# Kernel tuning notes

Measured on AMD Instinct MI355X. Metric: run time of the kernel, lower is better.

Reference implementation:

```python
import jax, jax.numpy as jnp
import numpy as np

D_MODEL = 1024
NUM_HEADS = 16
D_K = D_MODEL // NUM_HEADS
NEG = -1e9


def setup_inputs() -> dict:
    key = jax.random.key(0)
    ks = jax.random.split(key, 7)
    B, S = 2, 2048
    q = jax.random.normal(ks[0], (B, S, D_MODEL), dtype=jnp.float32)
    k = jax.random.normal(ks[1], (B, S, D_MODEL), dtype=jnp.float32)
    v = jax.random.normal(ks[2], (B, S, D_MODEL), dtype=jnp.float32)
    mask = jnp.ones((B, S), dtype=jnp.int32)
    # nn.Linear(d_model, d_model, bias=False): y = x @ W.T, W:[out,in]
    scale = 1.0 / np.sqrt(D_MODEL)
    Wq = jax.random.normal(ks[3], (D_MODEL, D_MODEL), dtype=jnp.float32) * scale
    Wk = jax.random.normal(ks[4], (D_MODEL, D_MODEL), dtype=jnp.float32) * scale
    Wv = jax.random.normal(ks[5], (D_MODEL, D_MODEL), dtype=jnp.float32) * scale
    Wo = jax.random.normal(ks[6], (D_MODEL, D_MODEL), dtype=jnp.float32) * scale
    return {"q": q, "k": k, "v": v, "mask": mask,
            "Wq": Wq, "Wk": Wk, "Wv": Wv, "Wo": Wo}


def _split_heads(x, B):
    # [B,S,D] -> [B,H,S,d_k]
    return x.reshape(B, -1, NUM_HEADS, D_K).transpose(0, 2, 1, 3)


def reference(q, k, v, mask, Wq, Wk, Wv, Wo):
    B = q.shape[0]
    qh = _split_heads(q @ Wq.T, B)
    kh = _split_heads(k @ Wk.T, B)
    vh = _split_heads(v @ Wv.T, B)
    # [B,H,Sq,Sk]
    scores = jnp.einsum('bhqd,bhkd->bhqk', qh, kh) / jnp.sqrt(jnp.float32(D_K))
    Sq, Sk = scores.shape[-2], scores.shape[-1]
    causal = jnp.triu(jnp.ones((Sq, Sk), dtype=bool), k=1)
    scores = jnp.where(causal[None, None], NEG, scores)
    pad = (mask[:, None, None, :] == 0)  # [B,1,1,Sk]
    scores = jnp.where(pad, NEG, scores)
    weights = jax.nn.softmax(scores, axis=-1)
    out = jnp.einsum('bhqk,bhkd->bhqd', weights, vh)
    out = out.transpose(0, 2, 1, 3).reshape(B, -1, D_MODEL)
    return out @ Wo.T
```

## Files before the change

### kernel.cpp

```cpp
#include <hip/hip_runtime.h>
#include <hip/hip_bf16.h>
#include <stdint.h>

using bf16 = __hip_bfloat16;
typedef __attribute__((ext_vector_type(8))) short short8;
typedef __attribute__((ext_vector_type(4))) float f32x4;
typedef __attribute__((ext_vector_type(16))) float f32x16;
typedef __attribute__((ext_vector_type(4))) float float4v;
typedef __attribute__((ext_vector_type(4))) unsigned short us4;
typedef __attribute__((ext_vector_type(4))) uint32_t u32x4;
typedef __attribute__((ext_vector_type(2))) uint32_t u32x2;

#define LDS_U32 __attribute__((address_space(3))) uint32_t
#define GLB_U32 __attribute__((address_space(1))) uint32_t

__device__ __forceinline__ unsigned short f2b(float f) {
  union { float f; uint32_t u; } x; x.f = f;
  uint32_t r = x.u + 0x7FFFu + ((x.u >> 16) & 1u);
  return (unsigned short)(r >> 16);
}

__global__ void cast_all(const float* __restrict__ q, const float* __restrict__ k,
                         const float* __restrict__ v, const float* __restrict__ Wq,
                         const float* __restrict__ Wk, const float* __restrict__ Wv,
                         const float* __restrict__ Wo,
                         bf16* __restrict__ qb, bf16* __restrict__ kb,
                         bf16* __restrict__ vb, bf16* __restrict__ Wqb,
                         bf16* __restrict__ Wkb, bf16* __restrict__ Wvb,
                         bf16* __restrict__ Wob) {
  const int NQ = 1 << 20;
  const int NW = 1 << 18;
  const int total = 3 * NQ + 4 * NW;
  for (int i = blockIdx.x * blockDim.x + threadIdx.x; i < total;
       i += gridDim.x * blockDim.x) {
    const float* s; bf16* d; int vi;
    if (i < 3 * NQ) {
      int a = i >> 20; vi = i & (NQ - 1);
      s = (a == 0) ? q : (a == 1) ? k : v;
      d = (a == 0) ? qb : (a == 1) ? kb : vb;
    } else {
      int j = i - 3 * NQ;
      int a = j >> 18; vi = j & (NW - 1);
      s = (a == 0) ? Wq : (a == 1) ? Wk : (a == 2) ? Wv : Wo;
      d = (a == 0) ? Wqb : (a == 1) ? Wkb : (a == 2) ? Wvb : Wob;
    }
    float4v x = ((const float4v*)s)[vi];
    us4 y;
    y.x = f2b(x.x); y.y = f2b(x.y); y.z = f2b(x.z); y.w = f2b(x.w);
    ((us4*)d)[vi] = y;
  }
}

__global__ __launch_bounds__(256, 2)
void qkv_proj(const bf16* __restrict__ Aq, const bf16* __restrict__ Ak,
              const bf16* __restrict__ Av,
              const bf16* __restrict__ Wq, const bf16* __restrict__ Wk,
              const bf16* __restrict__ Wv,
              bf16* __restrict__ Qh, bf16* __restrict__ KF, bf16* __restrict__ VF) {
  __shared__ bf16 Alds[128 * 64];
  __shared__ bf16 Blds[128 * 64];
  const int t = threadIdx.x, lane = t & 63, wave = t >> 6;
  const int l15 = lane & 15, l4 = lane >> 4;
  const int p = blockIdx.x;
  const int l = (p & 7) * 96 + (p >> 3);
  const int grp = l >> 3;
  const int n0 = (l & 7) * 128;
  const int seg = grp >> 5;
  const int m0 = (grp & 31) * 128;
  const bf16* A = (seg == 0) ? Aq : (seg == 1) ? Ak : Av;
  const bf16* B = (seg == 0) ? Wq : (seg == 1) ? Wk : Wv;
  const int K = 1024;
  const int wr = (wave >> 1) * 64, wc = (wave & 1) * 64;
  const float SCLE = 0.18033688011112042f;

  f32x4 acc[4][4] = {};

  for (int kt = 0; kt < K; kt += 64) {
#pragma unroll
    for (int i = 0; i < 4; ++i) {
      int f = i * 256 + t, row = f >> 3, csrc = (f & 7) ^ (row & 7);
      __builtin_amdgcn_global_load_lds(
          (const GLB_U32*)(A + (size_t)(m0 + row) * K + kt + csrc * 8),
          (LDS_U32*)(Alds + f * 8), 16, 0, 0);
      __builtin_amdgcn_global_load_lds(
          (const GLB_U32*)(B + (size_t)(n0 + row) * K + kt + csrc * 8),
          (LDS_U32*)(Blds + f * 8), 16, 0, 0);
    }
    __syncthreads();
#pragma unroll
    for (int ks = 0; ks < 2; ++ks) {
      short8 af[4], bfr[4];
#pragma unroll
      for (int mi = 0; mi < 4; ++mi) {
        int row = wr + mi * 16 + l15;
        int ch = (ks * 4 + l4) ^ (row & 7);
        af[mi] = *(const short8*)(Alds + row * 64 + ch * 8);
      }
#pragma unroll
      for (int ni = 0; ni < 4; ++ni) {
        int row = wc + ni * 16 + l15;
        int ch = (ks * 4 + l4) ^ (row & 7);
        bfr[ni] = *(const short8*)(Blds + row * 64 + ch * 8);
      }
#pragma unroll
      for (int mi = 0; mi < 4; ++mi)
#pragma unroll
        for (int ni = 0; ni < 4; ++ni)
          acc[mi][ni] = __builtin_amdgcn_mfma_f32_16x16x32_bf16(
              af[mi], bfr[ni], acc[mi][ni], 0, 0, 0);
    }
    __syncthreads();
  }

#pragma unroll
  for (int mi = 0; mi < 4; ++mi) {
#pragma unroll
    for (int ni = 0; ni < 4; ++ni) {
      int rbase = m0 + wr + mi * 16 + l4 * 4;
      int col = n0 + wc + ni * 16 + l15;
      if (seg == 0) {
        unsigned short* C = (unsigned short*)Qh;
#pragma unroll
        for (int r = 0; r < 4; ++r)
          C[(size_t)(rbase + r) * 1024 + col] = f2b(acc[mi][ni][r] * SCLE);
      } else if (seg == 1) {
        unsigned short* C = (unsigned short*)KF;
        int h = col >> 6, d = col & 63;
#pragma unroll
        for (int r = 0; r < 4; ++r) {
          int row = rbase + r;
          int b = row >> 11, s = row & 2047;
          size_t idx = (size_t)(b * 16 + h) * 131072 +
                       ((((s >> 5) * 4 + (d >> 4)) * 2 + ((d >> 3) & 1)) * 256) +
                       (s & 31) * 8 + (d & 7);
          C[idx] = f2b(acc[mi][ni][r]);
        }
      } else {
        unsigned short* C = (unsigned short*)VF;
        int h = col >> 6, d = col & 63;
        int row = rbase;
        int b = row >> 11, s = row & 2047;
        size_t idx = (size_t)(b * 16 + h) * 131072 +
                     (((((s >> 6) * 2 + ((d >> 5) & 1)) * 4 + ((s >> 4) & 3)) * 2 +
                       ((s >> 3) & 1)) * 256) +
                     (d & 31) * 8 + (s & 7);
        us4 y;
        y.x = f2b(acc[mi][ni][0]); y.y = f2b(acc[mi][ni][1]);
        y.z = f2b(acc[mi][ni][2]); y.w = f2b(acc[mi][ni][3]);
        *(us4*)(C + idx) = y;
      }
    }
  }
}

__global__ __launch_bounds__(256, 2)
void gemm_o(const bf16* __restrict__ A, const bf16* __restrict__ B,
            float* __restrict__ C) {
  __shared__ bf16 Alds[128 * 64];
  __shared__ bf16 Blds[64 * 64];
  const int t = threadIdx.x, lane = t & 63, wave = t >> 6;
  const int l15 = lane & 15, l4 = lane >> 4;
  const int p = blockIdx.x;
  const int l = (p & 7) * 64 + (p >> 3);
  const int m0 = (l >> 4) * 128;
  const int n0 = (l & 15) * 64;
  const int K = 1024;
  const int wr = (wave >> 1) * 64, wc = (wave & 1) * 32;

  f32x4 acc[4][2] = {};

  for (int kt = 0; kt < K; kt += 64) {
#pragma unroll
    for (int i = 0; i < 4; ++i) {
      int f = i * 256 + t, row = f >> 3, csrc = (f & 7) ^ (row & 7);
      __builtin_amdgcn_global_load_lds(
          (const GLB_U32*)(A + (size_t)(m0 + row) * K + kt + csrc * 8),
          (LDS_U32*)(Alds + f * 8), 16, 0, 0);
    }
#pragma unroll
    for (int i = 0; i < 2; ++i) {
      int f = i * 256 + t, row = f >> 3, csrc = (f & 7) ^ (row & 7);
      __builtin_amdgcn_global_load_lds(
          (const GLB_U32*)(B + (size_t)(n0 + row) * K + kt + csrc * 8),
          (LDS_U32*)(Blds + f * 8), 16, 0, 0);
    }
    __syncthreads();
#pragma unroll
    for (int ks = 0; ks < 2; ++ks) {
      short8 af[4], bfr[2];
#pragma unroll
      for (int mi = 0; mi < 4; ++mi) {
        int row = wr + mi * 16 + l15;
        int ch = (ks * 4 + l4) ^ (row & 7);
        af[mi] = *(const short8*)(Alds + row * 64 + ch * 8);
      }
#pragma unroll
      for (int ni = 0; ni < 2; ++ni) {
        int row = wc + ni * 16 + l15;
        int ch = (ks * 4 + l4) ^ (row & 7);
        bfr[ni] = *(const short8*)(Blds + row * 64 + ch * 8);
      }
#pragma unroll
      for (int mi = 0; mi < 4; ++mi)
#pragma unroll
        for (int ni = 0; ni < 2; ++ni)
          acc[mi][ni] = __builtin_amdgcn_mfma_f32_16x16x32_bf16(
              af[mi], bfr[ni], acc[mi][ni], 0, 0, 0);
    }
    __syncthreads();
  }

#pragma unroll
  for (int mi = 0; mi < 4; ++mi)
#pragma unroll
    for (int ni = 0; ni < 2; ++ni) {
      int rbase = m0 + wr + mi * 16 + l4 * 4;
      int col = n0 + wc + ni * 16 + l15;
#pragma unroll
      for (int r = 0; r < 4; ++r)
        C[(size_t)(rbase + r) * 1024 + col] = acc[mi][ni][r];
    }
}

__global__ __launch_bounds__(256, 2)
void attn_fwd(const bf16* __restrict__ Q, const bf16* __restrict__ KF,
              const bf16* __restrict__ VF, const int* __restrict__ mask,
              bf16* __restrict__ O) {
  const int lin = blockIdx.x;
  const int xcd = lin & 7, q8 = lin >> 3;
  const int bh = xcd + 8 * (q8 & 3), g = q8 >> 2;
  const int b = bh >> 4, h = bh & 15;
  const int wave = threadIdx.x >> 6, lane = threadIdx.x & 63;
  const int l31 = lane & 31, hi = lane >> 5;
  const int job = 2 * g + (wave >> 1);
  const int halfk = wave & 1, wp = wave >> 1;

  __shared__ float accL[2][64][33];
  __shared__ float mlL[2][64][2];

  const size_t bqk = (size_t)b * 2048 * 1024 + h * 64;
  const size_t fbase = (size_t)bh * 131072;

  for (int si = 0; si < 2; ++si) {
    const int s = si ? (63 - job) : job;
    const int q0 = 32 * s;
    const int T = (s >> 1) + 1;
    const int hsplit = (T + 1) >> 1;
    const int tstart = halfk ? hsplit : 0;
    const int tend = halfk ? T : hsplit;

    short8 qf[4];
#pragma unroll
    for (int s4 = 0; s4 < 4; ++s4)
      qf[s4] = *(const short8*)(Q + bqk + (size_t)(q0 + l31) * 1024 + 16 * s4 + 8 * hi);

    int anyz = 0;
    for (int i = tstart * 64 + lane; i < tend * 64; i += 64)
      anyz |= (mask[b * 2048 + i] == 0);
    const bool doMask = __any(anyz);

    f32x16 acc0 = {}, acc1 = {};
    float m = -1e30f, l = 0.f;

    short8 kf[2][4], kn[2][4], vf[2][4];
    if (tstart < tend) {
#pragma unroll
      for (int u = 0; u < 2; ++u)
#pragma unroll
        for (int s4 = 0; s4 < 4; ++s4)
          kf[u][s4] = *(const short8*)(KF + fbase +
              ((size_t)((2 * tstart + u) * 4 + s4) * 2 + hi) * 256 + l31 * 8);
    }

    for (int tt = tstart; tt < tend; ++tt) {
#pragma unroll
      for (int n = 0; n < 2; ++n)
#pragma unroll
        for (int tq = 0; tq < 4; ++tq)
          vf[n][tq] = *(const short8*)(VF + fbase +
              ((size_t)(((tt * 2 + n) * 4 + tq) * 2 + hi)) * 256 + l31 * 8);

      f32x16 s0 = {}, s1 = {};
      __builtin_amdgcn_s_setprio(1);
#pragma unroll
      for (int s4 = 0; s4 < 4; ++s4) {
        s0 = __builtin_amdgcn_mfma_f32_32x32x16_bf16(kf[0][s4], qf[s4], s0, 0, 0, 0);
        s1 = __builtin_amdgcn_mfma_f32_32x32x16_bf16(kf[1][s4], qf[s4], s1, 0, 0, 0);
      }
      __builtin_amdgcn_s_setprio(0);
      if (tt + 1 < tend) {
#pragma unroll
        for (int u = 0; u < 2; ++u)
#pragma unroll
          for (int s4 = 0; s4 < 4; ++s4)
            kn[u][s4] = *(const short8*)(KF + fbase +
                ((size_t)((2 * (tt + 1) + u) * 4 + s4) * 2 + hi) * 256 + l31 * 8);
      }

      float w[2][16];
#pragma unroll
      for (int p = 0; p < 16; ++p) { w[0][p] = s0[p]; w[1][p] = s1[p]; }

      if (doMask) {
        int mv = mask[b * 2048 + tt * 64 + lane];
        uint64_t bits = __ballot(mv != 0);
        uint64_t bs = bits >> (4 * hi);
#pragma unroll
        for (int u = 0; u < 2; ++u)
#pragma unroll
          for (int p = 0; p < 16; ++p)
            if (!((bs >> (32 * u + (p & 3) + 8 * (p >> 2))) & 1)) w[u][p] = -3e38f;
      }
      if (tt == T - 1) {
        int qr = 32 * (s & 1) + l31 - 4 * hi;
#pragma unroll
        for (int u = 0; u < 2; ++u)
#pragma unroll
          for (int p = 0; p < 16; ++p)
            if (32 * u + (p & 3) + 8 * (p >> 2) > qr) w[u][p] = -3e38f;
      }

      float tm = fmaxf(w[0][0], w[1][0]);
#pragma unroll
      for (int p = 1; p < 16; ++p) tm = fmaxf(tm, fmaxf(w[0][p], w[1][p]));
      tm = fmaxf(tm, __shfl_xor(tm, 32));

      if (!__all(tm <= m + 8.f)) {
        float mn = fmaxf(m, tm);
        float corr = __builtin_amdgcn_exp2f(m - mn);
        m = mn; l *= corr;
#pragma unroll
        for (int p = 0; p < 16; ++p) {
          float ct = __shfl(corr, (p & 3) + 8 * (p >> 2) + 4 * hi);
          acc0[p] *= ct; acc1[p] *= ct;
        }
      }

      float ts = 0.f;
#pragma unroll
      for (int u = 0; u < 2; ++u)
#pragma unroll
        for (int p = 0; p < 16; ++p) {
          float pv = __builtin_amdgcn_exp2f(w[u][p] - m);
          w[u][p] = pv; ts += pv;
        }
      ts += __shfl_xor(ts, 32);
      l += ts;

      uint32_t pkk[2][8];
#pragma unroll
      for (int u = 0; u < 2; ++u)
#pragma unroll
        for (int a = 0; a < 4; ++a)
#pragma unroll
          for (int w2 = 0; w2 < 2; ++w2) {
            uint32_t r;
            asm("v_cvt_pk_bf16_f32 %0, %1, %2"
                : "=v"(r) : "v"(w[u][4 * a + 2 * w2]), "v"(w[u][4 * a + 2 * w2 + 1]));
            pkk[u][2 * a + w2] = r;
          }

#pragma unroll
      for (int tq = 0; tq < 4; ++tq) {
        const int u = tq >> 1, alo = 2 * (tq & 1);
        uint32_t a0 = pkk[u][2 * alo + 0], b0 = pkk[u][2 * alo + 2];
        uint32_t a1 = pkk[u][2 * alo + 1], b1 = pkk[u][2 * alo + 3];
        asm("v_permlane32_swap_b32 %0, %1" : "+v"(a0), "+v"(b0));
        asm("v_permlane32_swap_b32 %0, %1" : "+v"(a1), "+v"(b1));
        u32x4 wv = {a0, a1, b0, b1};
        short8 paf = __builtin_bit_cast(short8, wv);
        __builtin_amdgcn_s_setprio(1);
        acc0 = __builtin_amdgcn_mfma_f32_32x32x16_bf16(paf, vf[0][tq], acc0, 0, 0, 0);
        acc1 = __builtin_amdgcn_mfma_f32_32x32x16_bf16(paf, vf[1][tq], acc1, 0, 0, 0);
        __builtin_amdgcn_s_setprio(0);
      }

#pragma unroll
      for (int u = 0; u < 2; ++u)
#pragma unroll
        for (int s4 = 0; s4 < 4; ++s4) kf[u][s4] = kn[u][s4];
    }

    if (halfk) {
#pragma unroll
      for (int p = 0; p < 16; ++p) {
        accL[wp][lane][p] = acc0[p];
        accL[wp][lane][16 + p] = acc1[p];
      }
      mlL[wp][lane][0] = m; mlL[wp][lane][1] = l;
    }
    __syncthreads();
    if (!halfk) {
      float mB = mlL[wp][lane][0], lB = mlL[wp][lane][1];
      float ms = fmaxf(m, mB);
      float cAr = __builtin_amdgcn_exp2f(m - ms);
      float cBr = __builtin_amdgcn_exp2f(mB - ms);
      float inv = 1.f / (cAr * l + cBr * lB);
      float fa = cAr * inv, fb = cBr * inv;
      unsigned short* Ou = (unsigned short*)O;
#pragma unroll
      for (int p = 0; p < 16; ++p) {
        int crow = (p & 3) + 8 * (p >> 2) + 4 * hi;
        float faT = __shfl(fa, crow);
        float fbT = __shfl(fb, crow);
        float o0 = acc0[p] * faT + accL[wp][lane][p] * fbT;
        float o1 = acc1[p] * faT + accL[wp][lane][16 + p] * fbT;
        size_t ro = (size_t)(b * 2048 + q0 + crow) * 1024 + h * 64;
        Ou[ro + l31] = f2b(o0);
        Ou[ro + 32 + l31] = f2b(o1);
      }
    }
    __syncthreads();
  }
}

extern "C" void kernel_launch(void* const* d_in, const int* in_sizes, int n_in,
                              void* d_out, int out_size, void* d_ws, size_t ws_size,
                              hipStream_t stream) {
  const float* q = (const float*)d_in[0];
  const float* k = (const float*)d_in[1];
  const float* v = (const float*)d_in[2];
  const int* mask = (const int*)d_in[3];
  const float* Wq = (const float*)d_in[4];
  const float* Wk = (const float*)d_in[5];
  const float* Wv = (const float*)d_in[6];
  const float* Wo = (const float*)d_in[7];
  float* out = (float*)d_out;

  const size_t NT = 4096 * 1024;
  const size_t NW = 1024 * 1024;
  bf16* p = (bf16*)d_ws;
  bf16* qb = p;  p += NT;
  bf16* kb = p;  p += NT;
  bf16* vb = p;  p += NT;
  bf16* Wqb = p; p += NW;
  bf16* Wkb = p; p += NW;
  bf16* Wvb = p; p += NW;
  bf16* Wob = p; p += NW;
  bf16* Qh = p;  p += NT;
  bf16* KF = p;  p += NT;
  bf16* VF = p;  p += NT;
  bf16* Oh = p;  p += NT;

  cast_all<<<2048, 256, 0, stream>>>(q, k, v, Wq, Wk, Wv, Wo,
                                     qb, kb, vb, Wqb, Wkb, Wvb, Wob);
  qkv_proj<<<768, 256, 0, stream>>>(qb, kb, vb, Wqb, Wkb, Wvb, Qh, KF, VF);
  attn_fwd<<<512, 256, 0, stream>>>(Qh, KF, VF, mask, Oh);
  gemm_o<<<512, 256, 0, stream>>>(Oh, Wob, out);
}
```

Baseline: 201.7 us.

## Split attention KV range across four waves per query block, doubling grid

Each attention block now serves a single query-tile job, and its four waves split that job's key range into quarters instead of two waves splitting it in halves. The partial softmax states are merged through shared memory by wave 0. The grid doubles to 1024 blocks and the launch bounds ask for four blocks per CU, which gives more parallelism and better load balance across the causal workload. It also replaces the row-max reduction with v_max3_f32. The costs are a larger LDS footprint, more merge work, and register pressure from the tighter occupancy target.

```diff
diff --git a/kernel.cpp b/kernel.cpp
--- a/kernel.cpp
+++ b/kernel.cpp
@@ -9,7 +9,6 @@
 typedef __attribute__((ext_vector_type(4))) float float4v;
 typedef __attribute__((ext_vector_type(4))) unsigned short us4;
 typedef __attribute__((ext_vector_type(4))) uint32_t u32x4;
-typedef __attribute__((ext_vector_type(2))) uint32_t u32x2;
 
 #define LDS_U32 __attribute__((address_space(3))) uint32_t
 #define GLB_U32 __attribute__((address_space(1))) uint32_t
@@ -18,6 +17,12 @@
   union { float f; uint32_t u; } x; x.f = f;
   uint32_t r = x.u + 0x7FFFu + ((x.u >> 16) & 1u);
   return (unsigned short)(r >> 16);
+}
+
+__device__ __forceinline__ float max3f(float a, float b, float c) {
+  float r;
+  asm("v_max3_f32 %0, %1, %2, %3" : "=v"(r) : "v"(a), "v"(b), "v"(c));
+  return r;
 }
 
 __global__ void cast_all(const float* __restrict__ q, const float* __restrict__ k,
@@ -222,21 +227,20 @@
     }
 }
 
-__global__ __launch_bounds__(256, 2)
+__global__ __launch_bounds__(256, 4)
 void attn_fwd(const bf16* __restrict__ Q, const bf16* __restrict__ KF,
               const bf16* __restrict__ VF, const int* __restrict__ mask,
               bf16* __restrict__ O) {
   const int lin = blockIdx.x;
-  const int xcd = lin & 7, q8 = lin >> 3;
-  const int bh = xcd + 8 * (q8 & 3), g = q8 >> 2;
+  const int xcd = lin & 7, rest = lin >> 3;
+  const int bh = xcd + 8 * (rest & 3);
+  const int job = rest >> 2;
   const int b = bh >> 4, h = bh & 15;
-  const int wave = threadIdx.x >> 6, lane = threadIdx.x & 63;
+  const int wq = threadIdx.x >> 6, lane = threadIdx.x & 63;
   const int l31 = lane & 31, hi = lane >> 5;
-  const int job = 2 * g + (wave >> 1);
-  const int halfk = wave & 1, wp = wave >> 1;
-
-  __shared__ float accL[2][64][33];
-  __shared__ float mlL[2][64][2];
+
+  __shared__ float accL[3][64][33];
+  __shared__ float mlL[3][64][2];
 
   const size_t bqk = (size_t)b * 2048 * 1024 + h * 64;
   const size_t fbase = (size_t)bh * 131072;
@@ -245,9 +249,8 @@
     const int s = si ? (63 - job) : job;
     const int q0 = 32 * s;
     const int T = (s >> 1) + 1;
-    const int hsplit = (T + 1) >> 1;
-    const int tstart = halfk ? hsplit : 0;
-    const int tend = halfk ? T : hsplit;
+    const int tstart = (T * wq) >> 2;
+    const int tend = (T * (wq + 1)) >> 2;
 
     short8 qf[4];
 #pragma unroll
@@ -320,9 +323,13 @@
             if (32 * u + (p & 3) + 8 * (p >> 2) > qr) w[u][p] = -3e38f;
       }
 
-      float tm = fmaxf(w[0][0], w[1][0]);
-#pragma unroll
-      for (int p = 1; p < 16; ++p) tm = fmaxf(tm, fmaxf(w[0][p], w[1][p]));
+      float tm = max3f(w[0][0], w[0][1], w[0][2]);
+#pragma unroll
+      for (int p = 3; p + 1 < 16; p += 2) tm = max3f(tm, w[0][p], w[0][p + 1]);
+      tm = max3f(tm, w[0][15], w[1][0]);
+#pragma unroll
+      for (int p = 1; p + 1 < 16; p += 2) tm = max3f(tm, w[1][p], w[1][p + 1]);
+      tm = fmaxf(tm, w[1][15]);
       tm = fmaxf(tm, __shfl_xor(tm, 32));
 
       if (!__all(tm <= m + 8.f)) {
@@ -381,30 +388,43 @@
         for (int s4 = 0; s4 < 4; ++s4) kf[u][s4] = kn[u][s4];
     }
 
-    if (halfk) {
+    if (wq) {
 #pragma unroll
       for (int p = 0; p < 16; ++p) {
-        accL[wp][lane][p] = acc0[p];
-        accL[wp][lane][16 + p] = acc1[p];
-      }
-      mlL[wp][lane][0] = m; mlL[wp][lane][1] = l;
-    }
-    __syncthreads();
-    if (!halfk) {
-      float mB = mlL[wp][lane][0], lB = mlL[wp][lane][1];
-      float ms = fmaxf(m, mB);
-      float cAr = __builtin_amdgcn_exp2f(m - ms);
-      float cBr = __builtin_amdgcn_exp2f(mB - ms);
-      float inv = 1.f / (cAr * l + cBr * lB);
-      float fa = cAr * inv, fb = cBr * inv;
+        accL[wq - 1][lane][p] = acc0[p];
+        accL[wq - 1][lane][16 + p] = acc1[p];
+      }
+      mlL[wq - 1][lane][0] = m; mlL[wq - 1][lane][1] = l;
+    }
+    __syncthreads();
+    if (wq == 0) {
+      float ms = m;
+#pragma unroll
+      for (int j = 0; j < 3; ++j) ms = fmaxf(ms, mlL[j][lane][0]);
+      float f0 = __builtin_amdgcn_exp2f(m - ms);
+      float lsum = f0 * l;
+      float fj[3];
+#pragma unroll
+      for (int j = 0; j < 3; ++j) {
+        fj[j] = __builtin_amdgcn_exp2f(mlL[j][lane][0] - ms);
+        lsum += fj[j] * mlL[j][lane][1];
+      }
+      float inv = 1.f / lsum;
+      f0 *= inv;
+#pragma unroll
+      for (int j = 0; j < 3; ++j) fj[j] *= inv;
       unsigned short* Ou = (unsigned short*)O;
 #pragma unroll
       for (int p = 0; p < 16; ++p) {
         int crow = (p & 3) + 8 * (p >> 2) + 4 * hi;
-        float faT = __shfl(fa, crow);
-        float fbT = __shfl(fb, crow);
-        float o0 = acc0[p] * faT + accL[wp][lane][p] * fbT;
-        float o1 = acc1[p] * faT + accL[wp][lane][16 + p] * fbT;
+        float w0 = __shfl(f0, crow);
+        float o0 = acc0[p] * w0, o1 = acc1[p] * w0;
+#pragma unroll
+        for (int j = 0; j < 3; ++j) {
+          float wj = __shfl(fj[j], crow);
+          o0 += accL[j][lane][p] * wj;
+          o1 += accL[j][lane][16 + p] * wj;
+        }
         size_t ro = (size_t)(b * 2048 + q0 + crow) * 1024 + h * 64;
         Ou[ro + l31] = f2b(o0);
         Ou[ro + 32 + l31] = f2b(o1);
@@ -445,6 +465,6 @@
   cast_all<<<2048, 256, 0, stream>>>(q, k, v, Wq, Wk, Wv, Wo,
                                      qb, kb, vb, Wqb, Wkb, Wvb, Wob);
   qkv_proj<<<768, 256, 0, stream>>>(qb, kb, vb, Wqb, Wkb, Wvb, Qh, KF, VF);
-  attn_fwd<<<512, 256, 0, stream>>>(Qh, KF, VF, mask, Oh);
+  attn_fwd<<<1024, 256, 0, stream>>>(Qh, KF, VF, mask, Oh);
   gemm_o<<<512, 256, 0, stream>>>(Oh, Wob, out);
 }
```

Result: slower. 357.1 us (+77.0%).
